# Kernel tuning notes

Measured on AMD Instinct MI355X. Metric: run time of the kernel, lower is better.

## Reference

```python
import jax, jax.numpy as jnp
import numpy as np

G, R = 2, 2          # heterogeneous graphs, meta-paths per node type
ND = NT = 3072       # drug / target node counts
NHEADS = 8
E = 100000           # DTI pairs
NEG = -1e9


def setup_inputs() -> dict:
    key = jax.random.key(0)
    ks = jax.random.split(key, 32)

    def rn(k, shape):
        return (jax.random.normal(k, shape) / np.sqrt(shape[0])).astype(jnp.float32)

    inp = {
        'x_drug': jax.random.normal(ks[0], (ND, 1024), dtype=jnp.float32),
        'x_target': jax.random.normal(ks[1], (NT, 1280), dtype=jnp.float32),
        'bias_drug': jnp.where(jax.random.uniform(ks[2], (G, R, ND, ND)) < 0.02, 0.0, NEG).astype(jnp.float32),
        'bias_target': jnp.where(jax.random.uniform(ks[3], (G, R, NT, NT)) < 0.02, 0.0, NEG).astype(jnp.float32),
        'edge_index': jax.random.randint(ks[4], (2, E), 0, ND, dtype=jnp.int64),
        'dnn_w1': rn(ks[5], (1024, 512)), 'dnn_b1': jnp.zeros((512,), jnp.float32),
        'dnn_w2': rn(ks[6], (512, 256)), 'dnn_b2': jnp.zeros((256,), jnp.float32),
        'dnn_w3': rn(ks[7], (256, 128)), 'dnn_b3': jnp.zeros((128,), jnp.float32),
        'tnn_w1': rn(ks[8], (1280, 512)), 'tnn_b1': jnp.zeros((512,), jnp.float32),
        'tnn_w2': rn(ks[9], (512, 256)), 'tnn_b2': jnp.zeros((256,), jnp.float32),
        'tnn_w3': rn(ks[10], (256, 128)), 'tnn_b3': jnp.zeros((128,), jnp.float32),
        'gat_w': rn(ks[11], (128, 16)),
        'gat_a1': rn(ks[12], (16, 1)),
        'gat_a2': rn(ks[13], (16, 1)),
        'att_w': rn(ks[14], (128, 128)), 'att_b': jnp.zeros((128,), jnp.float32),
        'att_u': rn(ks[15], (128,)),
        'a_omega': rn(ks[16], (128, 1)),
        'dec_w1': rn(ks[17], (256, 64)), 'dec_b1': jnp.zeros((64,), jnp.float32),
        'dec_w2': rn(ks[18], (64, 1)), 'dec_b2': jnp.zeros((1,), jnp.float32),
    }
    return inp


def reference(x_drug, x_target, bias_drug, bias_target, edge_index,
              dnn_w1, dnn_b1, dnn_w2, dnn_b2, dnn_w3, dnn_b3,
              tnn_w1, tnn_b1, tnn_w2, tnn_b2, tnn_w3, tnn_b3,
              gat_w, gat_a1, gat_a2, att_w, att_b, att_u, a_omega,
              dec_w1, dec_b1, dec_w2, dec_b2):

    def mlp3(x, w1, b1, w2, b2, w3, b3):  # feature NN (eval mode)
        h = jax.nn.relu(x @ w1 + b1)
        h = jax.nn.relu(h @ w2 + b2)
        return jax.nn.relu(h @ w3 + b3)

    def branch(feats, bias):
        # feats [N,128], bias [G,R,N,N]. Shared GAT layer + dropout off -> all heads identical.
        wh = feats @ gat_w                                                  # [N,16]
        e = jax.nn.leaky_relu(wh @ gat_a1 + (wh @ gat_a2).T, 0.2)           # [N,N]
        att = jax.nn.softmax(e[None, None] + bias, axis=-1)                 # [G,R,N,N]
        head = jax.nn.elu(jnp.einsum('grnm,md->grnd', att, wh))             # [G,R,N,16]
        multi = jnp.swapaxes(jnp.tile(head, (1, 1, 1, NHEADS)), 1, 2)       # [G,N,R,128]
        # semantic (meta-path) attention per graph
        v = jnp.tanh(multi @ att_w + att_b)                                 # [G,N,R,128]
        alphas = jax.nn.softmax(v @ att_u, axis=-1)                         # [G,N,R]
        per_graph = jnp.einsum('gnrh,gnr->gnh', multi, alphas)              # [G,N,128]
        # combine across heterogeneous graphs with a_omega + softmax(dim=0)
        w = jax.nn.softmax(jnp.mean(per_graph @ a_omega, axis=(1, 2)), axis=0)  # [G]
        return jnp.einsum('g,gnh->nh', w, per_graph)                        # [N,128]

    final_drug = branch(mlp3(x_drug, dnn_w1, dnn_b1, dnn_w2, dnn_b2, dnn_w3, dnn_b3), bias_drug)
    final_target = branch(mlp3(x_target, tnn_w1, tnn_b1, tnn_w2, tnn_b2, tnn_w3, tnn_b3), bias_target)

    # DTI decoder on edge pairs
    h = jnp.concatenate([final_drug[edge_index[0]], final_target[edge_index[1]]], axis=-1)  # [E,256]
    h = jax.nn.relu(h @ dec_w1 + dec_b1)
    return jax.nn.sigmoid(h @ dec_w2 + dec_b2).reshape(-1)
```

## Files before the change

### kernel.cpp

```cpp
#include <hip/hip_runtime.h>
#include <math.h>

#define ND 3072
#define EDG 100000
#define MAXE 128
#define ASL (128*8 + 16)
#define BSL (64*8 + 16)

typedef __attribute__((ext_vector_type(8))) short short8;
typedef __attribute__((ext_vector_type(4))) float f32x4;

enum : size_t {
  OFF_FEATD = 0,
  OFF_FEATT = OFF_FEATD + 393216,
  OFF_WHD   = OFF_FEATT + 393216,
  OFF_WHT   = OFF_WHD + 49152,
  OFF_S1D   = OFF_WHT + 49152,
  OFF_S2D   = OFF_S1D + 3072,
  OFF_S1T   = OFF_S2D + 3072,
  OFF_S2T   = OFF_S1T + 3072,
  OFF_HEADD = OFF_S2T + 3072,
  OFF_HEADT = OFF_HEADD + 196608,
  OFF_PGD   = OFF_HEADT + 196608,
  OFF_PGT   = OFF_PGD + 98304,
  OFF_F16D  = OFF_PGT + 98304,
  OFF_F16T  = OFF_F16D + 49152,
  OFF_AWS   = OFF_F16T + 49152,
  OFF_W1D   = OFF_AWS + 2048,
  OFF_W1T   = OFF_W1D + 1024,
  OFF_AOM   = OFF_W1T + 1024,
  OFF_DOTSD = OFF_AOM + 16,
  OFF_DOTST = OFF_DOTSD + 6144,
  OFF_GSUM  = OFF_DOTST + 6144,
  OFF_S2MD  = OFF_GSUM + 4,
  OFF_S2MT  = OFF_S2MD + 1,
  OFF_W1DH  = ((OFF_S2MT + 4) & ~(size_t)3),
  OFF_W1DL  = OFF_W1DH + 262144,
  OFF_W1TH  = OFF_W1DL + 262144,
  OFF_W1TL  = OFF_W1TH + 327680,
  OFF_W2DH  = OFF_W1TL + 327680,
  OFF_W2DL  = OFF_W2DH + 65536,
  OFF_W2TH  = OFF_W2DL + 65536,
  OFF_W2TL  = OFF_W2TH + 65536,
  OFF_W3DH  = OFF_W2TL + 65536,
  OFF_W3DL  = OFF_W3DH + 16384,
  OFF_W3TH  = OFF_W3DL + 16384,
  OFF_W3TL  = OFF_W3TH + 16384,
  OFF_XDH   = OFF_W3TL + 16384,
  OFF_XDL   = OFF_XDH + 1572864,
  OFF_XTH   = OFF_XDL + 1572864,
  OFF_XTL   = OFF_XTH + 1966080,
  OFF_H1DH  = OFF_XTL + 1966080,
  OFF_H1DL  = OFF_H1DH + 786432,
  OFF_H1TH  = OFF_H1DL + 786432,
  OFF_H1TL  = OFF_H1TH + 786432,
  OFF_H2DH  = OFF_H1TL + 786432,
  OFF_H2DL  = OFF_H2DH + 393216,
  OFF_H2TH  = OFF_H2DL + 393216,
  OFF_H2TL  = OFF_H2TH + 393216,
  WS_GRAND  = OFF_H2TL + 393216
};

__device__ __forceinline__ ushort f2bf(float f) {
  union { float f; unsigned u; } v; v.f = f;
  unsigned r = (v.u + 0x7fffu + ((v.u >> 16) & 1u)) >> 16;
  return (ushort)r;
}
__device__ __forceinline__ float bf2f(ushort h) {
  union { float f; unsigned u; } v; v.u = ((unsigned)h) << 16;
  return v.f;
}

__global__ __launch_bounds__(256) void prep_all(
    const float* __restrict__ w1d, const float* __restrict__ w1t,
    const float* __restrict__ w2d, const float* __restrict__ w2t,
    const float* __restrict__ w3d, const float* __restrict__ w3t,
    const float* __restrict__ xd,  const float* __restrict__ xt,
    const float* __restrict__ att_w, const float* __restrict__ dec_w1,
    const float* __restrict__ a_omega, float* __restrict__ ws)
{
  const int b = blockIdx.x, t = threadIdx.x;
  if (b < 736) {
    const float* W; ushort* hi; ushort* lo; int nsh, base;
    if (b < 256)      { W=w1d; hi=(ushort*)(ws+OFF_W1DH); lo=(ushort*)(ws+OFF_W1DL); nsh=9; base=0; }
    else if (b < 576) { W=w1t; hi=(ushort*)(ws+OFF_W1TH); lo=(ushort*)(ws+OFF_W1TL); nsh=9; base=256; }
    else if (b < 640) { W=w2d; hi=(ushort*)(ws+OFF_W2DH); lo=(ushort*)(ws+OFF_W2DL); nsh=8; base=576; }
    else if (b < 704) { W=w2t; hi=(ushort*)(ws+OFF_W2TH); lo=(ushort*)(ws+OFF_W2TL); nsh=8; base=640; }
    else if (b < 720) { W=w3d; hi=(ushort*)(ws+OFF_W3DH); lo=(ushort*)(ws+OFF_W3DL); nsh=7; base=704; }
    else              { W=w3t; hi=(ushort*)(ws+OFF_W3TH); lo=(ushort*)(ws+OFF_W3TL); nsh=7; base=720; }
    const int u = (b - base)*256 + t;
    const int k8 = u >> nsh;
    const int n  = u & ((1 << nsh) - 1);
    __align__(16) ushort h8[8], l8[8];
    #pragma unroll
    for (int j2 = 0; j2 < 8; ++j2) {
      float x = W[(size_t)(k8*8 + j2) * (1 << nsh) + n];
      ushort h = f2bf(x);
      h8[j2] = h; l8[j2] = f2bf(x - bf2f(h));
    }
    *(uint4*)&hi[(size_t)u*8] = *(const uint4*)h8;
    *(uint4*)&lo[(size_t)u*8] = *(const uint4*)l8;
  } else if (b < 7648) {
    const float* X; ushort* hi; ushort* lo; int base;
    if (b < 3808) { X=xd; hi=(ushort*)(ws+OFF_XDH); lo=(ushort*)(ws+OFF_XDL); base=736; }
    else          { X=xt; hi=(ushort*)(ws+OFF_XTH); lo=(ushort*)(ws+OFF_XTL); base=3808; }
    const size_t u = ((size_t)(b-base)*256 + t)*4;
    float4 v = *(const float4*)&X[u];
    ushort4 h, l;
    h.x=f2bf(v.x); l.x=f2bf(v.x-bf2f(h.x));
    h.y=f2bf(v.y); l.y=f2bf(v.y-bf2f(h.y));
    h.z=f2bf(v.z); l.z=f2bf(v.z-bf2f(h.z));
    h.w=f2bf(v.w); l.w=f2bf(v.w-bf2f(h.w));
    *(ushort4*)&hi[u] = h; *(ushort4*)&lo[u] = l;
  } else if (b == 7648) {
    float* aws = ws + OFF_AWS; float* aom = ws + OFF_AOM;
    for (int i = t; i < 2048; i += 256) {
      int d = i >> 7, o = i & 127;
      float sum = 0.f;
      #pragma unroll
      for (int tt = 0; tt < 8; ++tt) sum += att_w[(tt*16 + d)*128 + o];
      aws[i] = sum;
    }
    if (t < 16) {
      float sum = 0.f;
      #pragma unroll
      for (int tt = 0; tt < 8; ++tt) sum += a_omega[tt*16 + t];
      aom[t] = sum;
    }
  } else {
    float* W1d = ws + OFF_W1D; float* W1t = ws + OFF_W1T;
    for (int i = t; i < 1024; i += 256) {
      int d = i >> 6, o = i & 63;
      float sd = 0.f, st = 0.f;
      #pragma unroll
      for (int tt = 0; tt < 8; ++tt) {
        sd += dec_w1[(tt*16 + d)*64 + o];
        st += dec_w1[(128 + tt*16 + d)*64 + o];
      }
      W1d[i] = sd; W1t[i] = st;
    }
  }
}

template<int EPI>
__global__ __launch_bounds__(256) void mfma_gemm2(
    const ushort* __restrict__ A0h, const ushort* __restrict__ A0l,
    const ushort* __restrict__ B0h, const ushort* __restrict__ B0l,
    const float* __restrict__ b0, float* __restrict__ C0f,
    ushort* __restrict__ C0h, ushort* __restrict__ C0l,
    const ushort* __restrict__ A1h, const ushort* __restrict__ A1l,
    const ushort* __restrict__ B1h, const ushort* __restrict__ B1l,
    const float* __restrict__ b1, float* __restrict__ C1f,
    ushort* __restrict__ C1h, ushort* __restrict__ C1l,
    int N, int K0, int K1)
{
  __shared__ __align__(16) ushort Ah[8*ASL], Al[8*ASL];
  __shared__ __align__(16) ushort Bh[8*BSL], Bl[8*BSL];
  const int t = threadIdx.x;
  const int lane = t & 63, w = t >> 6;
  const int wr = w >> 1, wc = w & 1;
  const int l15 = lane & 15, l4 = lane >> 4;

  const int id = blockIdx.y * gridDim.x + blockIdx.x;
  const int xcd = id & 7;
  const int j = id >> 3;
  const int bx = j % gridDim.x;
  const int by = (j / gridDim.x) * 8 + xcd;
  const int half = by >= 24;
  const int row0 = (half ? by - 24 : by) << 7;
  const int col0 = bx << 6;
  const ushort* Ahi = half ? A1h : A0h; const ushort* Alo = half ? A1l : A0l;
  const ushort* Bhi = half ? B1h : B0h; const ushort* Blo = half ? B1l : B0l;
  const float* bias = half ? b1 : b0;
  float* Cf = half ? C1f : C0f;
  ushort* Chi = half ? C1h : C0h; ushort* Clo = half ? C1l : C0l;
  const int K = half ? K1 : K0;

  f32x4 acc[4][2] = {};

  const int arow = t >> 3;
  const int akc  = t & 7;
  const int bkc  = t >> 6;
  const int bcol = t & 63;

  uint4 sa0, sa1, sa2, sa3, sl0, sl1, sl2, sl3, sb0, sb1, sc0, sc1;

#define GLOAD(k0_) { \
    size_t g0 = (size_t)(row0 + arow      ) * K + (k0_) + (akc << 3); \
    size_t g1 = (size_t)(row0 + arow + 32 ) * K + (k0_) + (akc << 3); \
    size_t g2 = (size_t)(row0 + arow + 64 ) * K + (k0_) + (akc << 3); \
    size_t g3 = (size_t)(row0 + arow + 96 ) * K + (k0_) + (akc << 3); \
    sa0 = *(const uint4*)(Ahi + g0); sl0 = *(const uint4*)(Alo + g0); \
    sa1 = *(const uint4*)(Ahi + g1); sl1 = *(const uint4*)(Alo + g1); \
    sa2 = *(const uint4*)(Ahi + g2); sl2 = *(const uint4*)(Alo + g2); \
    sa3 = *(const uint4*)(Ahi + g3); sl3 = *(const uint4*)(Alo + g3); \
    size_t gb0 = ((size_t)(((k0_) >> 3) + bkc    ) * N + col0 + bcol) << 3; \
    size_t gb1 = ((size_t)(((k0_) >> 3) + bkc + 4) * N + col0 + bcol) << 3; \
    sb0 = *(const uint4*)(Bhi + gb0); sc0 = *(const uint4*)(Blo + gb0); \
    sb1 = *(const uint4*)(Bhi + gb1); sc1 = *(const uint4*)(Blo + gb1); \
  }

#define LDSW() { \
    int ao = akc * ASL + arow * 8; \
    *(uint4*)&Ah[ao        ] = sa0;  *(uint4*)&Al[ao        ] = sl0; \
    *(uint4*)&Ah[ao + 256  ] = sa1;  *(uint4*)&Al[ao + 256  ] = sl1; \
    *(uint4*)&Ah[ao + 512  ] = sa2;  *(uint4*)&Al[ao + 512  ] = sl2; \
    *(uint4*)&Ah[ao + 768  ] = sa3;  *(uint4*)&Al[ao + 768  ] = sl3; \
    int bo = bkc * BSL + bcol * 8; \
    *(uint4*)&Bh[bo          ] = sb0; *(uint4*)&Bl[bo          ] = sc0; \
    *(uint4*)&Bh[bo + 4*BSL  ] = sb1; *(uint4*)&Bl[bo + 4*BSL  ] = sc1; \
  }

  GLOAD(0);
  for (int k0 = 0; k0 < K; k0 += 64) {
    __syncthreads();
    LDSW();
    __syncthreads();
    if (k0 + 64 < K) GLOAD(k0 + 64);
    #pragma unroll
    for (int ks = 0; ks < 2; ++ks) {
      const int kch = (ks << 2) + l4;
      const int bbase = kch * BSL + ((wc << 5) + l15) * 8;
      short8 fb0 = *(const short8*)&Bh[bbase];
      short8 fb1 = *(const short8*)&Bh[bbase + 128];
      short8 gl0 = *(const short8*)&Bl[bbase];
      short8 gl1 = *(const short8*)&Bl[bbase + 128];
      #pragma unroll
      for (int m = 0; m < 4; ++m) {
        const int abase = kch * ASL + ((wr << 6) + (m << 4) + l15) * 8;
        short8 fa = *(const short8*)&Ah[abase];
        short8 fl = *(const short8*)&Al[abase];
        acc[m][0] = __builtin_amdgcn_mfma_f32_16x16x32_bf16(fa, fb0, acc[m][0], 0, 0, 0);
        acc[m][0] = __builtin_amdgcn_mfma_f32_16x16x32_bf16(fa, gl0, acc[m][0], 0, 0, 0);
        acc[m][0] = __builtin_amdgcn_mfma_f32_16x16x32_bf16(fl, fb0, acc[m][0], 0, 0, 0);
        acc[m][1] = __builtin_amdgcn_mfma_f32_16x16x32_bf16(fa, fb1, acc[m][1], 0, 0, 0);
        acc[m][1] = __builtin_amdgcn_mfma_f32_16x16x32_bf16(fa, gl1, acc[m][1], 0, 0, 0);
        acc[m][1] = __builtin_amdgcn_mfma_f32_16x16x32_bf16(fl, fb1, acc[m][1], 0, 0, 0);
      }
    }
  }
#undef GLOAD
#undef LDSW

  #pragma unroll
  for (int n = 0; n < 2; ++n) {
    int col = col0 + (wc << 5) + (n << 4) + l15;
    float bb = bias[col];
    #pragma unroll
    for (int m = 0; m < 4; ++m) {
      int rowb = row0 + (wr << 6) + (m << 4) + (l4 << 2);
      #pragma unroll
      for (int r = 0; r < 4; ++r) {
        float v = fmaxf(acc[m][n][r] + bb, 0.f);
        size_t d = (size_t)(rowb + r) * N + col;
        if (EPI == 0) {
          Cf[d] = v;
        } else {
          ushort h = f2bf(v);
          Chi[d] = h;
          Clo[d] = f2bf(v - bf2f(h));
        }
      }
    }
  }
}

__global__ __launch_bounds__(256) void wh_kernel(const float* __restrict__ featD,
    const float* __restrict__ featT,
    const float* __restrict__ gw, const float* __restrict__ ga1, const float* __restrict__ ga2,
    float* __restrict__ ws)
{
  __shared__ float W[128*16];
  __shared__ float A1[16], A2[16];
  const int t = threadIdx.x;
  const int half = blockIdx.x >= 192;
  const float* feat = half ? featT : featD;
  float* wh = ws + (half ? OFF_WHT : OFF_WHD);
  float* s1 = ws + (half ? OFF_S1T : OFF_S1D);
  float* s2 = ws + (half ? OFF_S2T : OFF_S2D);
  const int bid = half ? blockIdx.x - 192 : blockIdx.x;
  for (int i = t; i < 2048; i += 256) W[i] = gw[i];
  if (t < 16) { A1[t] = ga1[t]; A2[t] = ga2[t]; }
  __syncthreads();
  const int n = (bid << 4) + (t >> 4);
  const int d = t & 15;
  const float* f = feat + (size_t)n * 128;
  float acc = 0.f;
  #pragma unroll 8
  for (int k = 0; k < 128; ++k) acc += f[k] * W[k*16 + d];
  wh[(size_t)n*16 + d] = acc;
  float v1 = acc * A1[d], v2 = acc * A2[d];
  #pragma unroll
  for (int off = 8; off; off >>= 1) { v1 += __shfl_xor(v1, off); v2 += __shfl_xor(v2, off); }
  if (d == 0) { s1[n] = v1; s2[n] = v2; }
}

__global__ __launch_bounds__(256) void max_kernel(float* __restrict__ ws)
{
  const int t = threadIdx.x;
  const float* s2 = ws + (blockIdx.x ? OFF_S2T : OFF_S2D);
  float* out = ws + (blockIdx.x ? OFF_S2MT : OFF_S2MD);
  float m = -INFINITY;
  for (int i = t; i < ND; i += 256) m = fmaxf(m, s2[i]);
  #pragma unroll
  for (int off = 32; off; off >>= 1) m = fmaxf(m, __shfl_xor(m, off));
  __shared__ float red[4];
  if ((t & 63) == 0) red[t >> 6] = m;
  __syncthreads();
  if (t == 0) out[0] = fmaxf(fmaxf(red[0], red[1]), fmaxf(red[2], red[3]));
}

__global__ __launch_bounds__(256) void scan_kernel(const float* __restrict__ bias_d,
    const float* __restrict__ bias_t, float* __restrict__ ws)
{
  const int half = blockIdx.x >= 3072;
  const float* bias = half ? bias_t : bias_d;
  unsigned short* idx = (unsigned short*)(ws + (half ? OFF_H1TH : OFF_H1DH));
  int* cnts = (int*)(ws + (half ? OFF_H2TH : OFF_H2DH));
  const int bid = half ? blockIdx.x - 3072 : blockIdx.x;
  const int lane = threadIdx.x & 63;
  const int row = (bid << 2) + (threadIdx.x >> 6);
  const f32x4* brow = (const f32x4*)(bias + (size_t)row * ND);
  unsigned short* ei = idx + (size_t)row * MAXE;
  const unsigned long long ltmask = (1ull << lane) - 1ull;
  int cnt = 0;
  #pragma unroll 3
  for (int i = 0; i < ND/256; ++i) {
    const int j4 = lane + (i << 6);
    f32x4 b = __builtin_nontemporal_load(&brow[j4]);
    #pragma unroll
    for (int c = 0; c < 4; ++c) {
      float bv = b[c];
      bool e = bv > -1e8f;
      unsigned long long mask = __ballot(e);
      if (e) {
        int pos = cnt + __popcll(mask & ltmask);
        if (pos < MAXE) ei[pos] = (unsigned short)((j4 << 2) + c);
      }
      cnt += __popcll(mask);
    }
  }
  if (lane == 0) cnts[row] = cnt < MAXE ? cnt : MAXE;
}

__global__ __launch_bounds__(256) void acc_kernel(float* __restrict__ ws)
{
  const int half = blockIdx.x >= 3072;
  const unsigned short* idx = (const unsigned short*)(ws + (half ? OFF_H1TH : OFF_H1DH));
  const int* cnts = (const int*)(ws + (half ? OFF_H2TH : OFF_H2DH));
  const float* s1 = ws + (half ? OFF_S1T : OFF_S1D);
  const float* s2 = ws + (half ? OFF_S2T : OFF_S2D);
  const float* s2max = ws + (half ? OFF_S2MT : OFF_S2MD);
  const float* wh = ws + (half ? OFF_WHT : OFF_WHD);
  float* head = ws + (half ? OFF_HEADT : OFF_HEADD);
  const int bid = half ? blockIdx.x - 3072 : blockIdx.x;
  const int lane = threadIdx.x & 63;
  const int row = (bid << 2) + (threadIdx.x >> 6);
  const int n = row % ND;
  const int eg = lane >> 4, d = lane & 15;
  const float s1v = s1[n];
  float mn = s1v + s2max[0];
  mn = (mn >= 0.f) ? mn : 0.2f * mn;
  const unsigned short* ei = idx + (size_t)row * MAXE;
  const int cnt = cnts[row];
  float acc = 0.f, ss = 0.f;
  if (cnt > 0) {
    for (int slot = eg; slot < cnt; slot += 4) {
      int j = ei[slot];
      float x = s1v + s2[j];
      x = (x >= 0.f) ? x : 0.2f * x;
      float p = __expf(x - mn);
      ss += p;
      acc += p * wh[j*16 + d];
    }
  } else {
    for (int j = eg; j < ND; j += 4) {
      float x = s1v + s2[j];
      x = (x >= 0.f) ? x : 0.2f * x;
      float p = __expf(x - mn);
      ss += p;
      acc += p * wh[j*16 + d];
    }
  }
  acc += __shfl_xor(acc, 16); acc += __shfl_xor(acc, 32);
  ss  += __shfl_xor(ss, 16);  ss  += __shfl_xor(ss, 32);
  if (lane < 16) {
    float v = acc / ss;
    head[(size_t)row * 16 + lane] = (v > 0.f) ? v : expm1f(v);
  }
}

__global__ __launch_bounds__(256) void sem_kernel(const float* __restrict__ att_b,
    const float* __restrict__ att_u, float* __restrict__ ws)
{
  __shared__ float AWS[2048];
  __shared__ float AB[128], AU[128], AOM[16];
  __shared__ float hsh[2][2][16];
  __shared__ float wred[4][2];
  const int half = blockIdx.x >= 3072;
  const float* head = ws + (half ? OFF_HEADT : OFF_HEADD);
  float* pg = ws + (half ? OFF_PGT : OFF_PGD);
  float* dots = ws + (half ? OFF_DOTST : OFF_DOTSD);
  const float* aws = ws + OFF_AWS;
  const float* aom = ws + OFF_AOM;
  const int bid = half ? blockIdx.x - 3072 : blockIdx.x;
  const int t = threadIdx.x;
  for (int i = t; i < 2048; i += 256) AWS[i] = aws[i];
  if (t < 128) { AB[t] = att_b[t]; AU[t] = att_u[t]; }
  if (t < 16) AOM[t] = aom[t];
  const int grp = t >> 7, o = t & 127;
  const int gn = (bid << 1) + grp;
  const int g = gn / ND, n = gn % ND;
  if (o < 32) {
    int r = o >> 4, d = o & 15;
    hsh[grp][r][d] = head[((size_t)(g*2 + r) * ND + n) * 16 + d];
  }
  __syncthreads();
  #pragma unroll
  for (int r = 0; r < 2; ++r) {
    float a = AB[o];
    #pragma unroll
    for (int d = 0; d < 16; ++d) a += hsh[grp][r][d] * AWS[d*128 + o];
    float v = tanhf(a) * AU[o];
    #pragma unroll
    for (int off = 32; off; off >>= 1) v += __shfl_xor(v, off);
    if ((t & 63) == 0) wred[t >> 6][r] = v;
  }
  __syncthreads();
  float t0 = wred[grp*2][0] + wred[grp*2 + 1][0];
  float t1 = wred[grp*2][1] + wred[grp*2 + 1][1];
  float mx = fmaxf(t0, t1);
  float e0 = __expf(t0 - mx), e1 = __expf(t1 - mx);
  float inv = 1.f / (e0 + e1);
  float a0 = e0 * inv, a1 = e1 * inv;
  if (o < 16) {
    float pv = a0 * hsh[grp][0][o] + a1 * hsh[grp][1][o];
    pg[((size_t)g * ND + n) * 16 + o] = pv;
    float contrib = pv * AOM[o];
    #pragma unroll
    for (int off = 8; off; off >>= 1) contrib += __shfl_xor(contrib, off);
    if (o == 0) dots[(size_t)g * ND + n] = contrib;
  }
}

__global__ __launch_bounds__(256) void reduce_gsum(float* __restrict__ ws)
{
  const int b = blockIdx.x, t = threadIdx.x;
  const float* dots = ws + (b < 2 ? OFF_DOTSD : OFF_DOTST) + (size_t)(b & 1) * ND;
  float v = 0.f;
  for (int i = t; i < ND; i += 256) v += dots[i];
  __shared__ float red[4];
  #pragma unroll
  for (int off = 32; off; off >>= 1) v += __shfl_xor(v, off);
  if ((t & 63) == 0) red[t >> 6] = v;
  __syncthreads();
  if (t == 0) ws[OFF_GSUM + b] = red[0] + red[1] + red[2] + red[3];
}

__global__ __launch_bounds__(256) void finalize_kernel(float* __restrict__ ws)
{
  const int half = blockIdx.x >= 192;
  const float* pg = ws + (half ? OFF_PGT : OFF_PGD);
  const float* gsum = ws + OFF_GSUM + half*2;
  float* f16 = ws + (half ? OFF_F16T : OFF_F16D);
  const int bid = half ? blockIdx.x - 192 : blockIdx.x;
  float g0 = gsum[0] * (1.f/ND), g1 = gsum[1] * (1.f/ND);
  float mx = fmaxf(g0, g1);
  float e0 = __expf(g0 - mx), e1 = __expf(g1 - mx);
  float w0 = e0 / (e0 + e1), w1 = e1 / (e0 + e1);
  int i = bid * 256 + threadIdx.x;
  if (i < ND*16) f16[i] = w0 * pg[i] + w1 * pg[ND*16 + i];
}

__global__ __launch_bounds__(256) void dec_kernel(const int* __restrict__ ei,
    const float* __restrict__ ws, const float* __restrict__ b1,
    const float* __restrict__ w2, const float* __restrict__ b2,
    float* __restrict__ out)
{
  __shared__ float WdT[64][16], WtT[64][16];
  __shared__ float B1[64], W2s[64];
  const float* f16d = ws + OFF_F16D;
  const float* f16t = ws + OFF_F16T;
  const float* W1d = ws + OFF_W1D;
  const float* W1t = ws + OFF_W1T;
  const int t = threadIdx.x;
  for (int i = t; i < 1024; i += 256) {
    int d = i >> 6, o = i & 63;
    WdT[o][d] = W1d[i];
    WtT[o][d] = W1t[i];
  }
  if (t < 64) { B1[t] = b1[t]; W2s[t] = w2[t]; }
  __syncthreads();
  const int e = blockIdx.x * 256 + t;
  if (e >= EDG) return;
  const int i0 = ei[e], i1 = ei[EDG + e];
  const float4* pd = (const float4*)(f16d + (size_t)i0 * 16);
  const float4* pt = (const float4*)(f16t + (size_t)i1 * 16);
  float4 d0 = pd[0], d1 = pd[1], d2 = pd[2], d3 = pd[3];
  float4 e0 = pt[0], e1 = pt[1], e2 = pt[2], e3 = pt[3];
  float outv = b2[0];
  #pragma unroll 4
  for (int o = 0; o < 64; ++o) {
    const float4* wd = (const float4*)&WdT[o][0];
    const float4* wt = (const float4*)&WtT[o][0];
    float4 wd0 = wd[0], wd1 = wd[1], wd2 = wd[2], wd3 = wd[3];
    float4 wt0 = wt[0], wt1 = wt[1], wt2 = wt[2], wt3 = wt[3];
    float a = B1[o];
    a += d0.x*wd0.x + d0.y*wd0.y + d0.z*wd0.z + d0.w*wd0.w;
    a += d1.x*wd1.x + d1.y*wd1.y + d1.z*wd1.z + d1.w*wd1.w;
    a += d2.x*wd2.x + d2.y*wd2.y + d2.z*wd2.z + d2.w*wd2.w;
    a += d3.x*wd3.x + d3.y*wd3.y + d3.z*wd3.z + d3.w*wd3.w;
    a += e0.x*wt0.x + e0.y*wt0.y + e0.z*wt0.z + e0.w*wt0.w;
    a += e1.x*wt1.x + e1.y*wt1.y + e1.z*wt1.z + e1.w*wt1.w;
    a += e2.x*wt2.x + e2.y*wt2.y + e2.z*wt2.z + e2.w*wt2.w;
    a += e3.x*wt3.x + e3.y*wt3.y + e3.z*wt3.z + e3.w*wt3.w;
    a = fmaxf(a, 0.f);
    outv += a * W2s[o];
  }
  out[e] = 1.f / (1.f + __expf(-outv));
}

extern "C" void kernel_launch(void* const* d_in, const int* in_sizes, int n_in,
                              void* d_out, int out_size, void* d_ws, size_t ws_size,
                              hipStream_t stream)
{
  const float* x_drug   = (const float*)d_in[0];
  const float* x_target = (const float*)d_in[1];
  const float* bias_d   = (const float*)d_in[2];
  const float* bias_t   = (const float*)d_in[3];
  const int*   ei       = (const int*)d_in[4];
  const float* dnn_w1 = (const float*)d_in[5];  const float* dnn_b1 = (const float*)d_in[6];
  const float* dnn_w2 = (const float*)d_in[7];  const float* dnn_b2 = (const float*)d_in[8];
  const float* dnn_w3 = (const float*)d_in[9];  const float* dnn_b3 = (const float*)d_in[10];
  const float* tnn_w1 = (const float*)d_in[11]; const float* tnn_b1 = (const float*)d_in[12];
  const float* tnn_w2 = (const float*)d_in[13]; const float* tnn_b2 = (const float*)d_in[14];
  const float* tnn_w3 = (const float*)d_in[15]; const float* tnn_b3 = (const float*)d_in[16];
  const float* gat_w  = (const float*)d_in[17];
  const float* gat_a1 = (const float*)d_in[18];
  const float* gat_a2 = (const float*)d_in[19];
  const float* att_w  = (const float*)d_in[20];
  const float* att_b  = (const float*)d_in[21];
  const float* att_u  = (const float*)d_in[22];
  const float* a_omega= (const float*)d_in[23];
  const float* dec_w1 = (const float*)d_in[24]; const float* dec_b1 = (const float*)d_in[25];
  const float* dec_w2 = (const float*)d_in[26]; const float* dec_b2 = (const float*)d_in[27];
  float* out = (float*)d_out;
  float* ws = (float*)d_ws;

  ushort* w1dh = (ushort*)(ws + OFF_W1DH); ushort* w1dl = (ushort*)(ws + OFF_W1DL);
  ushort* w1th = (ushort*)(ws + OFF_W1TH); ushort* w1tl = (ushort*)(ws + OFF_W1TL);
  ushort* w2dh = (ushort*)(ws + OFF_W2DH); ushort* w2dl = (ushort*)(ws + OFF_W2DL);
  ushort* w2th = (ushort*)(ws + OFF_W2TH); ushort* w2tl = (ushort*)(ws + OFF_W2TL);
  ushort* w3dh = (ushort*)(ws + OFF_W3DH); ushort* w3dl = (ushort*)(ws + OFF_W3DL);
  ushort* w3th = (ushort*)(ws + OFF_W3TH); ushort* w3tl = (ushort*)(ws + OFF_W3TL);
  ushort* xdh  = (ushort*)(ws + OFF_XDH);  ushort* xdl  = (ushort*)(ws + OFF_XDL);
  ushort* xth  = (ushort*)(ws + OFF_XTH);  ushort* xtl  = (ushort*)(ws + OFF_XTL);
  ushort* h1dh = (ushort*)(ws + OFF_H1DH); ushort* h1dl = (ushort*)(ws + OFF_H1DL);
  ushort* h1th = (ushort*)(ws + OFF_H1TH); ushort* h1tl = (ushort*)(ws + OFF_H1TL);
  ushort* h2dh = (ushort*)(ws + OFF_H2DH); ushort* h2dl = (ushort*)(ws + OFF_H2DL);
  ushort* h2th = (ushort*)(ws + OFF_H2TH); ushort* h2tl = (ushort*)(ws + OFF_H2TL);
  float* featD = ws + OFF_FEATD;
  float* featT = ws + OFF_FEATT;

  prep_all<<<7650, 256, 0, stream>>>(dnn_w1, tnn_w1, dnn_w2, tnn_w2, dnn_w3, tnn_w3,
      x_drug, x_target, att_w, dec_w1, a_omega, ws);

  mfma_gemm2<1><<<dim3(8,48), 256, 0, stream>>>(
      xdh, xdl, w1dh, w1dl, dnn_b1, nullptr, h1dh, h1dl,
      xth, xtl, w1th, w1tl, tnn_b1, nullptr, h1th, h1tl, 512, 1024, 1280);
  mfma_gemm2<1><<<dim3(4,48), 256, 0, stream>>>(
      h1dh, h1dl, w2dh, w2dl, dnn_b2, nullptr, h2dh, h2dl,
      h1th, h1tl, w2th, w2tl, tnn_b2, nullptr, h2th, h2tl, 256, 512, 512);
  mfma_gemm2<0><<<dim3(2,48), 256, 0, stream>>>(
      h2dh, h2dl, w3dh, w3dl, dnn_b3, featD, nullptr, nullptr,
      h2th, h2tl, w3th, w3tl, tnn_b3, featT, nullptr, nullptr, 128, 256, 256);

  wh_kernel<<<384, 256, 0, stream>>>(featD, featT, gat_w, gat_a1, gat_a2, ws);
  max_kernel<<<2, 256, 0, stream>>>(ws);

  scan_kernel<<<6144, 256, 0, stream>>>(bias_d, bias_t, ws);
  acc_kernel<<<6144, 256, 0, stream>>>(ws);

  sem_kernel<<<6144, 256, 0, stream>>>(att_b, att_u, ws);
  reduce_gsum<<<4, 256, 0, stream>>>(ws);
  finalize_kernel<<<384, 256, 0, stream>>>(ws);

  dec_kernel<<<(EDG + 255) / 256, 256, 0, stream>>>(ei, ws, dec_b1, dec_w2, dec_b2, out);
}
```

Baseline: 215.6 us.

## Fuse bias scan with attention accumulation and use smaller GEMM row tiles

Merges the separate scan kernel (which compacted edge indices from the dense bias rows) and the accumulate kernel into one kernel. The new kernel streams each bias row and directly accumulates the softmax-weighted wh rows for present edges, then reduces across the wave with shuffles. This removes one launch and the index round-trip through global memory, and also drops the MAXE truncation, at the cost of divergent per-lane work and a larger shuffle reduction. It also templates the MFMA GEMM on row-tile size and uses 64-row tiles for the two smaller layers, doubling their block count to improve occupancy.

```diff
diff --git a/kernel.cpp b/kernel.cpp
--- a/kernel.cpp
+++ b/kernel.cpp
@@ -3,8 +3,6 @@
 
 #define ND 3072
 #define EDG 100000
-#define MAXE 128
-#define ASL (128*8 + 16)
 #define BSL (64*8 + 16)
 
 typedef __attribute__((ext_vector_type(8))) short short8;
@@ -142,7 +140,7 @@
   }
 }
 
-template<int EPI>
+template<int BM, int EPI>
 __global__ __launch_bounds__(256) void mfma_gemm2(
     const ushort* __restrict__ A0h, const ushort* __restrict__ A0l,
     const ushort* __restrict__ B0h, const ushort* __restrict__ B0l,
@@ -154,7 +152,10 @@
     ushort* __restrict__ C1h, ushort* __restrict__ C1l,
     int N, int K0, int K1)
 {
-  __shared__ __align__(16) ushort Ah[8*ASL], Al[8*ASL];
+  constexpr int ASLT = BM*8 + 16;
+  constexpr int NP   = 3072 / BM;
+  constexpr int AI   = BM / 32;
+  __shared__ __align__(16) ushort Ah[8*ASLT], Al[8*ASLT];
   __shared__ __align__(16) ushort Bh[8*BSL], Bl[8*BSL];
   const int t = threadIdx.x;
   const int lane = t & 63, w = t >> 6;
@@ -166,8 +167,8 @@
   const int j = id >> 3;
   const int bx = j % gridDim.x;
   const int by = (j / gridDim.x) * 8 + xcd;
-  const int half = by >= 24;
-  const int row0 = (half ? by - 24 : by) << 7;
+  const int half = by >= NP;
+  const int row0 = (half ? by - NP : by) * BM;
   const int col0 = bx << 6;
   const ushort* Ahi = half ? A1h : A0h; const ushort* Alo = half ? A1l : A0l;
   const ushort* Bhi = half ? B1h : B0h; const ushort* Blo = half ? B1l : B0l;
@@ -176,7 +177,7 @@
   ushort* Chi = half ? C1h : C0h; ushort* Clo = half ? C1l : C0l;
   const int K = half ? K1 : K0;
 
-  f32x4 acc[4][2] = {};
+  f32x4 acc[AI][2] = {};
 
   const int arow = t >> 3;
   const int akc  = t & 7;
@@ -186,14 +187,13 @@
   uint4 sa0, sa1, sa2, sa3, sl0, sl1, sl2, sl3, sb0, sb1, sc0, sc1;
 
 #define GLOAD(k0_) { \
-    size_t g0 = (size_t)(row0 + arow      ) * K + (k0_) + (akc << 3); \
-    size_t g1 = (size_t)(row0 + arow + 32 ) * K + (k0_) + (akc << 3); \
-    size_t g2 = (size_t)(row0 + arow + 64 ) * K + (k0_) + (akc << 3); \
-    size_t g3 = (size_t)(row0 + arow + 96 ) * K + (k0_) + (akc << 3); \
-    sa0 = *(const uint4*)(Ahi + g0); sl0 = *(const uint4*)(Alo + g0); \
-    sa1 = *(const uint4*)(Ahi + g1); sl1 = *(const uint4*)(Alo + g1); \
-    sa2 = *(const uint4*)(Ahi + g2); sl2 = *(const uint4*)(Alo + g2); \
-    sa3 = *(const uint4*)(Ahi + g3); sl3 = *(const uint4*)(Alo + g3); \
+    size_t g0 = (size_t)(row0 + arow) * K + (k0_) + (akc << 3); \
+    sa0 = *(const uint4*)(Ahi + g0);                     sl0 = *(const uint4*)(Alo + g0); \
+    sa1 = *(const uint4*)(Ahi + g0 + 32*(size_t)K);      sl1 = *(const uint4*)(Alo + g0 + 32*(size_t)K); \
+    if (AI > 2) { \
+      sa2 = *(const uint4*)(Ahi + g0 + 64*(size_t)K);    sl2 = *(const uint4*)(Alo + g0 + 64*(size_t)K); \
+      sa3 = *(const uint4*)(Ahi + g0 + 96*(size_t)K);    sl3 = *(const uint4*)(Alo + g0 + 96*(size_t)K); \
+    } \
     size_t gb0 = ((size_t)(((k0_) >> 3) + bkc    ) * N + col0 + bcol) << 3; \
     size_t gb1 = ((size_t)(((k0_) >> 3) + bkc + 4) * N + col0 + bcol) << 3; \
     sb0 = *(const uint4*)(Bhi + gb0); sc0 = *(const uint4*)(Blo + gb0); \
@@ -201,14 +201,16 @@
   }
 
 #define LDSW() { \
-    int ao = akc * ASL + arow * 8; \
-    *(uint4*)&Ah[ao        ] = sa0;  *(uint4*)&Al[ao        ] = sl0; \
-    *(uint4*)&Ah[ao + 256  ] = sa1;  *(uint4*)&Al[ao + 256  ] = sl1; \
-    *(uint4*)&Ah[ao + 512  ] = sa2;  *(uint4*)&Al[ao + 512  ] = sl2; \
-    *(uint4*)&Ah[ao + 768  ] = sa3;  *(uint4*)&Al[ao + 768  ] = sl3; \
+    int ao = akc * ASLT + arow * 8; \
+    *(uint4*)&Ah[ao      ] = sa0;  *(uint4*)&Al[ao      ] = sl0; \
+    *(uint4*)&Ah[ao + 256] = sa1;  *(uint4*)&Al[ao + 256] = sl1; \
+    if (AI > 2) { \
+      *(uint4*)&Ah[ao + 512] = sa2;  *(uint4*)&Al[ao + 512] = sl2; \
+      *(uint4*)&Ah[ao + 768] = sa3;  *(uint4*)&Al[ao + 768] = sl3; \
+    } \
     int bo = bkc * BSL + bcol * 8; \
-    *(uint4*)&Bh[bo          ] = sb0; *(uint4*)&Bl[bo          ] = sc0; \
-    *(uint4*)&Bh[bo + 4*BSL  ] = sb1; *(uint4*)&Bl[bo + 4*BSL  ] = sc1; \
+    *(uint4*)&Bh[bo        ] = sb0; *(uint4*)&Bl[bo        ] = sc0; \
+    *(uint4*)&Bh[bo + 4*BSL] = sb1; *(uint4*)&Bl[bo + 4*BSL] = sc1; \
   }
 
   GLOAD(0);
@@ -226,8 +228,8 @@
       short8 gl0 = *(const short8*)&Bl[bbase];
       short8 gl1 = *(const short8*)&Bl[bbase + 128];
       #pragma unroll
-      for (int m = 0; m < 4; ++m) {
-        const int abase = kch * ASL + ((wr << 6) + (m << 4) + l15) * 8;
+      for (int m = 0; m < AI; ++m) {
+        const int abase = kch * ASLT + (wr*(BM/2) + (m << 4) + l15) * 8;
         short8 fa = *(const short8*)&Ah[abase];
         short8 fl = *(const short8*)&Al[abase];
         acc[m][0] = __builtin_amdgcn_mfma_f32_16x16x32_bf16(fa, fb0, acc[m][0], 0, 0, 0);
@@ -247,8 +249,8 @@
     int col = col0 + (wc << 5) + (n << 4) + l15;
     float bb = bias[col];
     #pragma unroll
-    for (int m = 0; m < 4; ++m) {
-      int rowb = row0 + (wr << 6) + (m << 4) + (l4 << 2);
+    for (int m = 0; m < AI; ++m) {
+      int rowb = row0 + wr*(BM/2) + (m << 4) + (l4 << 2);
       #pragma unroll
       for (int r = 0; r < 4; ++r) {
         float v = fmaxf(acc[m][n][r] + bb, 0.f);
@@ -310,44 +312,11 @@
   if (t == 0) out[0] = fmaxf(fmaxf(red[0], red[1]), fmaxf(red[2], red[3]));
 }
 
-__global__ __launch_bounds__(256) void scan_kernel(const float* __restrict__ bias_d,
+__global__ __launch_bounds__(256) void scanacc_kernel(const float* __restrict__ bias_d,
     const float* __restrict__ bias_t, float* __restrict__ ws)
 {
   const int half = blockIdx.x >= 3072;
   const float* bias = half ? bias_t : bias_d;
-  unsigned short* idx = (unsigned short*)(ws + (half ? OFF_H1TH : OFF_H1DH));
-  int* cnts = (int*)(ws + (half ? OFF_H2TH : OFF_H2DH));
-  const int bid = half ? blockIdx.x - 3072 : blockIdx.x;
-  const int lane = threadIdx.x & 63;
-  const int row = (bid << 2) + (threadIdx.x >> 6);
-  const f32x4* brow = (const f32x4*)(bias + (size_t)row * ND);
-  unsigned short* ei = idx + (size_t)row * MAXE;
-  const unsigned long long ltmask = (1ull << lane) - 1ull;
-  int cnt = 0;
-  #pragma unroll 3
-  for (int i = 0; i < ND/256; ++i) {
-    const int j4 = lane + (i << 6);
-    f32x4 b = __builtin_nontemporal_load(&brow[j4]);
-    #pragma unroll
-    for (int c = 0; c < 4; ++c) {
-      float bv = b[c];
-      bool e = bv > -1e8f;
-      unsigned long long mask = __ballot(e);
-      if (e) {
-        int pos = cnt + __popcll(mask & ltmask);
-        if (pos < MAXE) ei[pos] = (unsigned short)((j4 << 2) + c);
-      }
-      cnt += __popcll(mask);
-    }
-  }
-  if (lane == 0) cnts[row] = cnt < MAXE ? cnt : MAXE;
-}
-
-__global__ __launch_bounds__(256) void acc_kernel(float* __restrict__ ws)
-{
-  const int half = blockIdx.x >= 3072;
-  const unsigned short* idx = (const unsigned short*)(ws + (half ? OFF_H1TH : OFF_H1DH));
-  const int* cnts = (const int*)(ws + (half ? OFF_H2TH : OFF_H2DH));
   const float* s1 = ws + (half ? OFF_S1T : OFF_S1D);
   const float* s2 = ws + (half ? OFF_S2T : OFF_S2D);
   const float* s2max = ws + (half ? OFF_S2MT : OFF_S2MD);
@@ -357,35 +326,74 @@
   const int lane = threadIdx.x & 63;
   const int row = (bid << 2) + (threadIdx.x >> 6);
   const int n = row % ND;
-  const int eg = lane >> 4, d = lane & 15;
   const float s1v = s1[n];
   float mn = s1v + s2max[0];
   mn = (mn >= 0.f) ? mn : 0.2f * mn;
-  const unsigned short* ei = idx + (size_t)row * MAXE;
-  const int cnt = cnts[row];
-  float acc = 0.f, ss = 0.f;
-  if (cnt > 0) {
-    for (int slot = eg; slot < cnt; slot += 4) {
-      int j = ei[slot];
-      float x = s1v + s2[j];
+  const f32x4* brow = (const f32x4*)(bias + (size_t)row * ND);
+
+  float ss = 0.f;
+  int cnt = 0;
+  f32x4 a0 = {0,0,0,0}, a1 = {0,0,0,0}, a2 = {0,0,0,0}, a3 = {0,0,0,0};
+  #pragma unroll 4
+  for (int i = 0; i < ND/256; ++i) {
+    const int j4 = lane + (i << 6);
+    f32x4 b = __builtin_nontemporal_load(&brow[j4]);
+    #pragma unroll
+    for (int c = 0; c < 4; ++c) {
+      if (b[c] > -1e8f) {
+        int jj = (j4 << 2) + c;
+        float x = s1v + s2[jj];
+        x = (x >= 0.f) ? x : 0.2f * x;
+        float p = __expf(x - mn);
+        ss += p;
+        const f32x4* whr = (const f32x4*)(wh + (size_t)jj * 16);
+        a0 += p * whr[0]; a1 += p * whr[1]; a2 += p * whr[2]; a3 += p * whr[3];
+        ++cnt;
+      }
+    }
+  }
+  #pragma unroll
+  for (int off = 32; off; off >>= 1) {
+    ss += __shfl_xor(ss, off);
+    cnt += __shfl_xor(cnt, off);
+    a0[0] += __shfl_xor(a0[0], off); a0[1] += __shfl_xor(a0[1], off);
+    a0[2] += __shfl_xor(a0[2], off); a0[3] += __shfl_xor(a0[3], off);
+    a1[0] += __shfl_xor(a1[0], off); a1[1] += __shfl_xor(a1[1], off);
+    a1[2] += __shfl_xor(a1[2], off); a1[3] += __shfl_xor(a1[3], off);
+    a2[0] += __shfl_xor(a2[0], off); a2[1] += __shfl_xor(a2[1], off);
+    a2[2] += __shfl_xor(a2[2], off); a2[3] += __shfl_xor(a2[3], off);
+    a3[0] += __shfl_xor(a3[0], off); a3[1] += __shfl_xor(a3[1], off);
+    a3[2] += __shfl_xor(a3[2], off); a3[3] += __shfl_xor(a3[3], off);
+  }
+  if (cnt == 0) {
+    ss = 0.f;
+    a0 = (f32x4){0,0,0,0}; a1 = a0; a2 = a0; a3 = a0;
+    for (int jj = lane; jj < ND; jj += 64) {
+      float x = s1v + s2[jj];
       x = (x >= 0.f) ? x : 0.2f * x;
       float p = __expf(x - mn);
       ss += p;
-      acc += p * wh[j*16 + d];
-    }
-  } else {
-    for (int j = eg; j < ND; j += 4) {
-      float x = s1v + s2[j];
-      x = (x >= 0.f) ? x : 0.2f * x;
-      float p = __expf(x - mn);
-      ss += p;
-      acc += p * wh[j*16 + d];
-    }
-  }
-  acc += __shfl_xor(acc, 16); acc += __shfl_xor(acc, 32);
-  ss  += __shfl_xor(ss, 16);  ss  += __shfl_xor(ss, 32);
+      const f32x4* whr = (const f32x4*)(wh + (size_t)jj * 16);
+      a0 += p * whr[0]; a1 += p * whr[1]; a2 += p * whr[2]; a3 += p * whr[3];
+    }
+    #pragma unroll
+    for (int off = 32; off; off >>= 1) {
+      ss += __shfl_xor(ss, off);
+      a0[0] += __shfl_xor(a0[0], off); a0[1] += __shfl_xor(a0[1], off);
+      a0[2] += __shfl_xor(a0[2], off); a0[3] += __shfl_xor(a0[3], off);
+      a1[0] += __shfl_xor(a1[0], off); a1[1] += __shfl_xor(a1[1], off);
+      a1[2] += __shfl_xor(a1[2], off); a1[3] += __shfl_xor(a1[3], off);
+      a2[0] += __shfl_xor(a2[0], off); a2[1] += __shfl_xor(a2[1], off);
+      a2[2] += __shfl_xor(a2[2], off); a2[3] += __shfl_xor(a2[3], off);
+      a3[0] += __shfl_xor(a3[0], off); a3[1] += __shfl_xor(a3[1], off);
+      a3[2] += __shfl_xor(a3[2], off); a3[3] += __shfl_xor(a3[3], off);
+    }
+  }
   if (lane < 16) {
-    float v = acc / ss;
+    const int q = lane >> 2, rs = lane & 3;
+    f32x4 av = (q == 0) ? a0 : ((q == 1) ? a1 : ((q == 2) ? a2 : a3));
+    float v = (rs == 0) ? av[0] : ((rs == 1) ? av[1] : ((rs == 2) ? av[2] : av[3]));
+    v /= ss;
     head[(size_t)row * 16 + lane] = (v > 0.f) ? v : expm1f(v);
   }
 }
@@ -565,21 +573,20 @@
   prep_all<<<7650, 256, 0, stream>>>(dnn_w1, tnn_w1, dnn_w2, tnn_w2, dnn_w3, tnn_w3,
       x_drug, x_target, att_w, dec_w1, a_omega, ws);
 
-  mfma_gemm2<1><<<dim3(8,48), 256, 0, stream>>>(
+  mfma_gemm2<128,1><<<dim3(8,48), 256, 0, stream>>>(
       xdh, xdl, w1dh, w1dl, dnn_b1, nullptr, h1dh, h1dl,
       xth, xtl, w1th, w1tl, tnn_b1, nullptr, h1th, h1tl, 512, 1024, 1280);
-  mfma_gemm2<1><<<dim3(4,48), 256, 0, stream>>>(
+  mfma_gemm2<64,1><<<dim3(4,96), 256, 0, stream>>>(
       h1dh, h1dl, w2dh, w2dl, dnn_b2, nullptr, h2dh, h2dl,
       h1th, h1tl, w2th, w2tl, tnn_b2, nullptr, h2th, h2tl, 256, 512, 512);
-  mfma_gemm2<0><<<dim3(2,48), 256, 0, stream>>>(
+  mfma_gemm2<64,0><<<dim3(2,96), 256, 0, stream>>>(
       h2dh, h2dl, w3dh, w3dl, dnn_b3, featD, nullptr, nullptr,
       h2th, h2tl, w3th, w3tl, tnn_b3, featT, nullptr, nullptr, 128, 256, 256);
 
   wh_kernel<<<384, 256, 0, stream>>>(featD, featT, gat_w, gat_a1, gat_a2, ws);
   max_kernel<<<2, 256, 0, stream>>>(ws);
 
-  scan_kernel<<<6144, 256, 0, stream>>>(bias_d, bias_t, ws);
-  acc_kernel<<<6144, 256, 0, stream>>>(ws);
+  scanacc_kernel<<<6144, 256, 0, stream>>>(bias_d, bias_t, ws);
 
   sem_kernel<<<6144, 256, 0, stream>>>(att_b, att_u, ws);
   reduce_gsum<<<4, 256, 0, stream>>>(ws);
```

Result: slower. 281.2 us (+30.4%).
